# Optimization experiments

Measured on AMD Instinct MI355X. Metric: run time of the kernel, lower is better.

## Reference

```python
import jax, jax.numpy as jnp
import numpy as np

HIDDEN = 1024
N_HEADS = 16
HEAD_DIM = HIDDEN // N_HEADS


def setup_inputs() -> dict:
    key = jax.random.key(0)
    ks = jax.random.split(key, 10)
    s = 0.02
    return {
        "x": jax.random.normal(ks[0], (2, 2048, HIDDEN), dtype=jnp.float32),
        "wq_w": jax.random.normal(ks[1], (HEAD_DIM, HEAD_DIM), dtype=jnp.float32) * s,
        "wq_b": jax.random.normal(ks[2], (HEAD_DIM,), dtype=jnp.float32) * s,
        "wk_w": jax.random.normal(ks[3], (HEAD_DIM, HEAD_DIM), dtype=jnp.float32) * s,
        "wk_b": jax.random.normal(ks[4], (HEAD_DIM,), dtype=jnp.float32) * s,
        "wv_w": jax.random.normal(ks[5], (HEAD_DIM, HEAD_DIM), dtype=jnp.float32) * s,
        "wv_b": jax.random.normal(ks[6], (HEAD_DIM,), dtype=jnp.float32) * s,
        "wo_w": jax.random.normal(ks[7], (HIDDEN, HIDDEN), dtype=jnp.float32) * s,
        "wo_b": jax.random.normal(ks[8], (HIDDEN,), dtype=jnp.float32) * s,
    }


def reference(x, wq_w, wq_b, wk_w, wk_b, wv_w, wv_b, wo_w, wo_b):
    B, S, _ = x.shape
    # Faithful to torch: plain reshape (view), NOT a transpose-based head split.
    xh = x.reshape(B, N_HEADS, S, HEAD_DIM)  # [B,H,S,D]
    # torch Linear: y = x @ W.T + b
    Q = jnp.einsum('bhsd,ed->bhse', xh, wq_w) + wq_b
    K = jnp.einsum('bhsd,ed->bhse', xh, wk_w) + wk_b
    V = jnp.einsum('bhsd,ed->bhse', xh, wv_w) + wv_b
    scale = 1.0 / jnp.sqrt(jnp.float32(HEAD_DIM))
    scores = jnp.einsum('bhqd,bhkd->bhqk', Q, K) * scale  # [B,H,S,S]
    attn = jax.nn.softmax(scores, axis=-1)
    ctx = jnp.einsum('bhqk,bhkd->bhqd', attn, V)  # [B,H,S,D]
    out = ctx.reshape(B, S, HIDDEN)
    return out @ wo_w.T + wo_b
```

## Files before the change

### kernel.cpp

```cpp
#include <hip/hip_runtime.h>
#include <hip/hip_bf16.h>

#define SEQ 2048
#define BHCOUNT 32
#define NROWS (BHCOUNT*SEQ)

typedef unsigned short u16;
typedef unsigned int u32;
using bf16x8 = __attribute__((ext_vector_type(8))) short;
using f32x4  = __attribute__((ext_vector_type(4))) float;

__device__ __forceinline__ float bf2f(u16 h) {
    return __uint_as_float(((u32)h) << 16);
}
__device__ __forceinline__ u16 f2bf(float f) {
    u32 u = __float_as_uint(f);
    u32 r = (u + 0x7FFFu + ((u >> 16) & 1u)) >> 16;
    return (u16)r;
}
__device__ __forceinline__ float fexp2(float x) {
    float r; asm("v_exp_f32 %0, %1" : "=v"(r) : "v"(x)); return r;
}

__device__ __forceinline__ void gload16(const u16* g, u16* l) {
    __builtin_amdgcn_global_load_lds(
        (const __attribute__((address_space(1))) u32*)g,
        (__attribute__((address_space(3))) u32*)l, 16, 0, 0);
}

__device__ __forceinline__ void cvt8(const float* src, float sc, u16* o) {
    float4 a = *(const float4*)src;
    float4 b = *(const float4*)(src + 4);
    o[0]=f2bf(a.x*sc); o[1]=f2bf(a.y*sc); o[2]=f2bf(a.z*sc); o[3]=f2bf(a.w*sc);
    o[4]=f2bf(b.x*sc); o[5]=f2bf(b.y*sc); o[6]=f2bf(b.z*sc); o[7]=f2bf(b.w*sc);
}

__global__ __launch_bounds__(256) void qkv_kernel(
    const float* __restrict__ x,
    const float* __restrict__ wq, const float* __restrict__ bq,
    const float* __restrict__ wk, const float* __restrict__ bk,
    const float* __restrict__ wv, const float* __restrict__ bv,
    u16* __restrict__ Q, u16* __restrict__ K, u16* __restrict__ Vg)
{
    __shared__ u16 xs[128*64];
    __shared__ u16 ws[192*64];
    __shared__ float bs[192];
    const int t = threadIdx.x;
    const int wid = t >> 6, lane = t & 63;
    const int ln = lane & 15, g4 = lane >> 4;
    const int blk = blockIdx.x;
    const int m0 = blk * 128;
    const int bh = blk >> 4;
    const int ktg0 = (blk & 15) * 2;
    const float qscale = 0.125f * 1.44269504f;

    #pragma unroll
    for (int c = 0; c < 6; ++c) {
        int slot = c*256 + t;
        int row = slot >> 3, ks = slot & 7;
        const float* wsrc = (c < 2) ? wq : (c < 4) ? wk : wv;
        float sc = (c < 2) ? qscale : 1.f;
        u16 o[8];
        cvt8(&wsrc[(row & 63)*64 + ks*8], sc, o);
        *(uint4*)&ws[row*64 + ((ks ^ (row & 7)) << 3)] = *(uint4*)o;
    }
    #pragma unroll
    for (int c = 0; c < 4; ++c) {
        int slot = c*256 + t;
        int row = slot >> 3, ks = slot & 7;
        u16 o[8];
        cvt8(&x[(size_t)(m0 + row)*64 + ks*8], 1.f, o);
        *(uint4*)&xs[row*64 + ((ks ^ (row & 7)) << 3)] = *(uint4*)o;
    }
    if (t < 192) {
        int p = t >> 6, e = t & 63;
        bs[t] = (p == 0) ? bq[e]*qscale : (p == 1) ? bk[e] : bv[e];
    }
    __syncthreads();

    bf16x8 af[2][2];
    #pragma unroll
    for (int mf = 0; mf < 2; ++mf)
        #pragma unroll
        for (int kf = 0; kf < 2; ++kf) {
            int arow = wid*32 + mf*16 + ln;
            af[mf][kf] = *(const bf16x8*)&xs[arow*64 + (((kf*4 + g4) ^ (arow & 7)) << 3)];
        }

    #pragma unroll
    for (int p = 0; p < 2; ++p) {
        bf16x8 bfr[4][2];
        #pragma unroll
        for (int nt = 0; nt < 4; ++nt)
            #pragma unroll
            for (int kf = 0; kf < 2; ++kf) {
                int brow = p*64 + nt*16 + ln;
                bfr[nt][kf] = *(const bf16x8*)&ws[brow*64 + (((kf*4 + g4) ^ (ln & 7)) << 3)];
            }
        f32x4 acc[2][4];
        #pragma unroll
        for (int mf = 0; mf < 2; ++mf)
            #pragma unroll
            for (int nt = 0; nt < 4; ++nt) acc[mf][nt] = (f32x4){0.f,0.f,0.f,0.f};
        #pragma unroll
        for (int kf = 0; kf < 2; ++kf)
            #pragma unroll
            for (int mf = 0; mf < 2; ++mf)
                #pragma unroll
                for (int nt = 0; nt < 4; ++nt)
                    acc[mf][nt] = __builtin_amdgcn_mfma_f32_16x16x32_bf16(
                        af[mf][kf], bfr[nt][kf], acc[mf][nt], 0, 0, 0);
        u16* dst = p ? K : Q;
        #pragma unroll
        for (int mf = 0; mf < 2; ++mf)
            #pragma unroll
            for (int nt = 0; nt < 4; ++nt) {
                float bv4 = bs[p*64 + nt*16 + ln];
                #pragma unroll
                for (int r = 0; r < 4; ++r)
                    dst[(size_t)(m0 + wid*32 + mf*16 + g4*4 + r)*64 + nt*16 + ln]
                        = f2bf(acc[mf][nt][r] + bv4);
            }
    }

    bf16x8 wvf[4][2];
    #pragma unroll
    for (int et = 0; et < 4; ++et)
        #pragma unroll
        for (int kf = 0; kf < 2; ++kf) {
            int brow = 128 + et*16 + ln;
            wvf[et][kf] = *(const bf16x8*)&ws[brow*64 + (((kf*4 + g4) ^ (ln & 7)) << 3)];
        }
    f32x4 vacc[4][2];
    #pragma unroll
    for (int et = 0; et < 4; ++et)
        #pragma unroll
        for (int st = 0; st < 2; ++st) vacc[et][st] = (f32x4){0.f,0.f,0.f,0.f};
    #pragma unroll
    for (int kf = 0; kf < 2; ++kf)
        #pragma unroll
        for (int et = 0; et < 4; ++et)
            #pragma unroll
            for (int st = 0; st < 2; ++st)
                vacc[et][st] = __builtin_amdgcn_mfma_f32_16x16x32_bf16(
                    wvf[et][kf], af[st][kf], vacc[et][st], 0, 0, 0);

    __syncthreads();
    u16* vstage = xs;
    #pragma unroll
    for (int et = 0; et < 4; ++et)
        #pragma unroll
        for (int st = 0; st < 2; ++st)
            #pragma unroll
            for (int r = 0; r < 4; ++r) {
                int e = et*16 + g4*4 + r;
                int s = wid*32 + st*16 + ln;
                vstage[e*128 + ((s + 2*e) & 127)] = f2bf(vacc[et][st][r] + bs[128 + e]);
            }
    __syncthreads();

    #pragma unroll
    for (int c = 0; c < 8; ++c) {
        int j = c*256 + t;
        int kt2 = j >> 10, within = j & 1023;
        int ee = within >> 4, kp0 = (within & 15) * 4;
        int sbase = ((kp0 & 4) << 3) | ((kp0 & 32) >> 1) | ((kp0 & 24) >> 1);
        u16 o[4];
        #pragma unroll
        for (int i = 0; i < 4; ++i)
            o[i] = vstage[ee*128 + ((kt2*64 + sbase + i + 2*ee) & 127)];
        *(uint2*)&Vg[((size_t)bh*32 + ktg0 + kt2)*4096 + ee*64 + kp0] = *(uint2*)o;
    }
}

__device__ __forceinline__ void qkt_tile(
    const u16* Ks, const int (&foff)[4][2], const bf16x8 (&qf)[2], f32x4 (&sacc)[4])
{
    __builtin_amdgcn_s_setprio(1);
    #pragma unroll
    for (int nt = 0; nt < 4; ++nt) {
        sacc[nt] = (f32x4){0.f, 0.f, 0.f, 0.f};
        #pragma unroll
        for (int kf = 0; kf < 2; ++kf)
            sacc[nt] = __builtin_amdgcn_mfma_f32_16x16x32_bf16(
                *(const bf16x8*)&Ks[foff[nt][kf]], qf[kf], sacc[nt], 0, 0, 0);
    }
    __builtin_amdgcn_s_setprio(0);
}

__device__ __forceinline__ void sm_pv(
    f32x4 (&sacc)[4], f32x4 (&oacc)[4], f32x4& lacc,
    const u16* Vts, const int (&foff)[4][2], const bf16x8& ones)
{
    #pragma unroll
    for (int nt = 0; nt < 4; ++nt)
        #pragma unroll
        for (int r = 0; r < 4; ++r)
            sacc[nt][r] = fexp2(sacc[nt][r]);

    union PU { u32 w[4]; bf16x8 v; } pu0, pu1;
    asm("v_cvt_pk_bf16_f32 %0, %1, %2" : "=v"(pu0.w[0]) : "v"(sacc[0][0]), "v"(sacc[0][1]));
    asm("v_cvt_pk_bf16_f32 %0, %1, %2" : "=v"(pu0.w[1]) : "v"(sacc[0][2]), "v"(sacc[0][3]));
    asm("v_cvt_pk_bf16_f32 %0, %1, %2" : "=v"(pu0.w[2]) : "v"(sacc[2][0]), "v"(sacc[2][1]));
    asm("v_cvt_pk_bf16_f32 %0, %1, %2" : "=v"(pu0.w[3]) : "v"(sacc[2][2]), "v"(sacc[2][3]));
    asm("v_cvt_pk_bf16_f32 %0, %1, %2" : "=v"(pu1.w[0]) : "v"(sacc[1][0]), "v"(sacc[1][1]));
    asm("v_cvt_pk_bf16_f32 %0, %1, %2" : "=v"(pu1.w[1]) : "v"(sacc[1][2]), "v"(sacc[1][3]));
    asm("v_cvt_pk_bf16_f32 %0, %1, %2" : "=v"(pu1.w[2]) : "v"(sacc[3][0]), "v"(sacc[3][1]));
    asm("v_cvt_pk_bf16_f32 %0, %1, %2" : "=v"(pu1.w[3]) : "v"(sacc[3][2]), "v"(sacc[3][3]));
    bf16x8 pf[2] = { pu0.v, pu1.v };

    __builtin_amdgcn_s_setprio(1);
    #pragma unroll
    for (int dt = 0; dt < 4; ++dt)
        #pragma unroll
        for (int kf = 0; kf < 2; ++kf)
            oacc[dt] = __builtin_amdgcn_mfma_f32_16x16x32_bf16(
                pf[kf], *(const bf16x8*)&Vts[foff[dt][kf]], oacc[dt], 0, 0, 0);
    #pragma unroll
    for (int kf = 0; kf < 2; ++kf)
        lacc = __builtin_amdgcn_mfma_f32_16x16x32_bf16(pf[kf], ones, lacc, 0, 0, 0);
    __builtin_amdgcn_s_setprio(0);
}

__global__ __launch_bounds__(512) void attn_kernel(
    const u16* __restrict__ Q, const u16* __restrict__ K,
    const u16* __restrict__ Vg, u16* __restrict__ ctx)
{
    __shared__ u16 Kls[3*4096];
    __shared__ u16 Vls[3*4096];

    const int t = threadIdx.x;
    const int wid = t >> 6, lane = t & 63;
    const int ln = lane & 15, g4 = lane >> 4;
    const int bh = blockIdx.y;
    const size_t base   = (size_t)bh * SEQ * 64;
    const size_t vgbase = (size_t)bh * 32 * 4096;
    const int q0 = blockIdx.x * 128 + wid * 16;

    int goff;
    {
        int row = t >> 3, ks = t & 7;
        goff = row*64 + ((ks ^ (row & 7)) << 3);
    }
    const int ldst = wid * 512;

    int foff[4][2];
    #pragma unroll
    for (int nt = 0; nt < 4; ++nt)
        #pragma unroll
        for (int kf = 0; kf < 2; ++kf) {
            int frow = nt*16 + ln;
            foff[nt][kf] = frow*64 + (((kf*4 + g4) ^ (frow & 7)) << 3);
        }

    bf16x8 qf[2];
    #pragma unroll
    for (int kf = 0; kf < 2; ++kf)
        qf[kf] = *(const bf16x8*)&Q[base + (size_t)(q0 + ln)*64 + kf*32 + g4*8];

    bf16x8 ones;
    #pragma unroll
    for (int i = 0; i < 8; ++i) ones[i] = (short)0x3F80;

    f32x4 oacc[4];
    #pragma unroll
    for (int i = 0; i < 4; ++i) oacc[i] = (f32x4){0.f, 0.f, 0.f, 0.f};
    f32x4 lacc = (f32x4){0.f, 0.f, 0.f, 0.f};

    gload16(&K [base   + goff], &Kls[ldst]);
    gload16(&Vg[vgbase + goff], &Vls[ldst]);
    gload16(&K [base   + 4096 + goff], &Kls[4096 + ldst]);
    gload16(&Vg[vgbase + 4096 + goff], &Vls[4096 + ldst]);
    const u16* kptr = &K [base   + 2*4096 + goff];
    const u16* vptr = &Vg[vgbase + 2*4096 + goff];
    __syncthreads();

    f32x4 sA[4], sB[4];
    qkt_tile(&Kls[0], foff, qf, sA);

    #define ABODY(PREV, CUR, SP, SC, SN, STG)                               \
        do {                                                                \
            __syncthreads();                                                \
            if (STG) {                                                      \
                gload16(kptr, &Kls[(SN)*4096 + ldst]);                      \
                gload16(vptr, &Vls[(SN)*4096 + ldst]);                      \
                kptr += 4096; vptr += 4096;                                 \
            }                                                               \
            qkt_tile(&Kls[(SC)*4096], foff, qf, CUR);                       \
            sm_pv(PREV, oacc, lacc, &Vls[(SP)*4096], foff, ones);           \
        } while (0)

    for (int c = 0; c < 5; ++c) {
        ABODY(sA, sB, 0, 1, 2, 1);
        ABODY(sB, sA, 1, 2, 0, 1);
        ABODY(sA, sB, 2, 0, 1, 1);
        ABODY(sB, sA, 0, 1, 2, 1);
        ABODY(sA, sB, 1, 2, 0, 1);
        ABODY(sB, sA, 2, 0, 1, 1);
    }
    ABODY(sA, sB, 0, 1, 2, 0);
    sm_pv(sB, oacc, lacc, &Vls[1*4096], foff, ones);

    #undef ABODY

    #pragma unroll
    for (int r = 0; r < 4; ++r) {
        float inv = 1.f / lacc[r];
        size_t row = base + (size_t)(q0 + g4*4 + r)*64;
        #pragma unroll
        for (int dt = 0; dt < 4; ++dt)
            ctx[row + dt*16 + ln] = f2bf(oacc[dt][r] * inv);
    }
}

__global__ __launch_bounds__(256) void wconv_kernel(
    const float* __restrict__ wo, u16* __restrict__ wob_t)
{
    int g = blockIdx.x*256 + threadIdx.x;
    int tile = g >> 9, within = g & 511;
    int row = within >> 3, ks = within & 7;
    int cb = tile >> 4, kt = tile & 15;
    u16 o[8];
    cvt8(&wo[(size_t)(cb*64 + row)*1024 + kt*64 + ks*8], 1.f, o);
    *(uint4*)&wob_t[(size_t)g*8] = *(uint4*)o;
}

__global__ __launch_bounds__(256) void oproj_kernel(
    const u16* __restrict__ ctx, const u16* __restrict__ wob_t,
    const float* __restrict__ bo, float* __restrict__ out)
{
    __shared__ u16 As[128*64];
    __shared__ u16 Bs[64*64];
    const int t = threadIdx.x;
    const int wid = t >> 6, lane = t & 63;
    const int ln = lane & 15, g4 = lane >> 4;
    const int wr = wid >> 1, wc = wid & 1;
    const int rb = blockIdx.x, cb = blockIdx.y;
    const int m0 = rb * 128;

    f32x4 acc[4][2];
    #pragma unroll
    for (int mf = 0; mf < 4; ++mf)
        #pragma unroll
        for (int nf = 0; nf < 2; ++nf)
            acc[mf][nf] = (f32x4){0.f, 0.f, 0.f, 0.f};

    for (int kt = 0; kt < 16; ++kt) {
        const u16* bsrc = &wob_t[(size_t)(cb*16 + kt) * 4096];
        __syncthreads();
        #pragma unroll
        for (int c = 0; c < 4; ++c) {
            int sA = t + c*256;
            int row = sA >> 3, ks = sA & 7;
            *(uint4*)&As[row*64 + ((ks ^ (row & 7)) << 3)] =
                *(const uint4*)&ctx[(size_t)(m0 + row)*1024 + kt*64 + ks*8];
        }
        #pragma unroll
        for (int c = 0; c < 2; ++c) {
            int sB = t + c*256;
            int row = sB >> 3, ks = sB & 7;
            *(uint4*)&Bs[row*64 + ((ks ^ (row & 7)) << 3)] = *(const uint4*)&bsrc[sB*8];
        }
        __syncthreads();

        #pragma unroll
        for (int kf = 0; kf < 2; ++kf) {
            bf16x8 af[4], bfr[2];
            #pragma unroll
            for (int mf = 0; mf < 4; ++mf) {
                int arow = wr*64 + mf*16 + ln;
                af[mf] = *(const bf16x8*)&As[arow*64 + (((kf*4 + g4) ^ (arow & 7)) << 3)];
            }
            #pragma unroll
            for (int nf = 0; nf < 2; ++nf) {
                int brow = wc*32 + nf*16 + ln;
                bfr[nf] = *(const bf16x8*)&Bs[brow*64 + (((kf*4 + g4) ^ (brow & 7)) << 3)];
            }
            #pragma unroll
            for (int mf = 0; mf < 4; ++mf)
                #pragma unroll
                for (int nf = 0; nf < 2; ++nf)
                    acc[mf][nf] = __builtin_amdgcn_mfma_f32_16x16x32_bf16(af[mf], bfr[nf], acc[mf][nf], 0, 0, 0);
        }
    }

    #pragma unroll
    for (int mf = 0; mf < 4; ++mf)
        #pragma unroll
        for (int r = 0; r < 4; ++r) {
            int m = m0 + wr*64 + mf*16 + g4*4 + r;
            #pragma unroll
            for (int nf = 0; nf < 2; ++nf) {
                int col = cb*64 + wc*32 + nf*16 + ln;
                out[(size_t)m*1024 + col] = acc[mf][nf][r] + bo[col];
            }
        }
}

extern "C" void kernel_launch(void* const* d_in, const int* in_sizes, int n_in,
                              void* d_out, int out_size, void* d_ws, size_t ws_size,
                              hipStream_t stream) {
    (void)in_sizes; (void)n_in; (void)out_size; (void)ws_size;
    const float* x  = (const float*)d_in[0];
    const float* wq = (const float*)d_in[1];
    const float* bq = (const float*)d_in[2];
    const float* wk = (const float*)d_in[3];
    const float* bk = (const float*)d_in[4];
    const float* wv = (const float*)d_in[5];
    const float* bv = (const float*)d_in[6];
    const float* wo = (const float*)d_in[7];
    const float* bo = (const float*)d_in[8];
    float* out = (float*)d_out;

    u16* Qb  = (u16*)d_ws;
    u16* Kb  = Qb + (size_t)NROWS*64;
    u16* Vgb = Kb + (size_t)NROWS*64;
    u16* ctx = Vgb + (size_t)NROWS*64;
    u16* wob_t = Qb;

    qkv_kernel<<<dim3(NROWS/128), 256, 0, stream>>>(x, wq, bq, wk, bk, wv, bv, Qb, Kb, Vgb);
    attn_kernel<<<dim3(16, 32), 512, 0, stream>>>(Qb, Kb, Vgb, ctx);
    wconv_kernel<<<dim3(512), 256, 0, stream>>>(wo, wob_t);
    oproj_kernel<<<dim3(32, 16), 256, 0, stream>>>(ctx, wob_t, bo, out);
}
```

Measured before the change: 74.81 us.

## Fold wo conversion into QKV launch and double-buffer oproj with async LDS loads

The separate wconv kernel is merged into the QKV kernel as 512 extra blocks, which removes one launch. Its output buffer moves to its own workspace region after ctx, so it is no longer aliased with Q. The output-projection GEMM now uses double-buffered LDS filled by global_load_lds direct loads with a pre-swizzled global addressing. The next k-tile is prefetched while MFMAs run on the current one, and s_setprio is raised around the math. The cost is twice the LDS in oproj and extra workspace for wob_t.

Result: faster. 71.40 us (-4.6%).

```diff
diff --git a/kernel.cpp b/kernel.cpp
--- a/kernel.cpp
+++ b/kernel.cpp
@@ -35,17 +35,31 @@
     o[4]=f2bf(b.x*sc); o[5]=f2bf(b.y*sc); o[6]=f2bf(b.z*sc); o[7]=f2bf(b.w*sc);
 }
 
-__global__ __launch_bounds__(256) void qkv_kernel(
+__global__ __launch_bounds__(256) void qkv_wconv_kernel(
     const float* __restrict__ x,
     const float* __restrict__ wq, const float* __restrict__ bq,
     const float* __restrict__ wk, const float* __restrict__ bk,
     const float* __restrict__ wv, const float* __restrict__ bv,
-    u16* __restrict__ Q, u16* __restrict__ K, u16* __restrict__ Vg)
+    const float* __restrict__ wo,
+    u16* __restrict__ Q, u16* __restrict__ K, u16* __restrict__ Vg,
+    u16* __restrict__ wob_t)
 {
     __shared__ u16 xs[128*64];
     __shared__ u16 ws[192*64];
     __shared__ float bs[192];
     const int t = threadIdx.x;
+
+    if (blockIdx.x >= 512) {
+        int g = (blockIdx.x - 512)*256 + t;
+        int tile = g >> 9, within = g & 511;
+        int row = within >> 3, ks = within & 7;
+        int cb = tile >> 4, kt = tile & 15;
+        u16 o[8];
+        cvt8(&wo[(size_t)(cb*64 + row)*1024 + kt*64 + ks*8], 1.f, o);
+        *(uint4*)&wob_t[(size_t)g*8] = *(uint4*)o;
+        return;
+    }
+
     const int wid = t >> 6, lane = t & 63;
     const int ln = lane & 15, g4 = lane >> 4;
     const int blk = blockIdx.x;
@@ -313,24 +327,12 @@
     }
 }
 
-__global__ __launch_bounds__(256) void wconv_kernel(
-    const float* __restrict__ wo, u16* __restrict__ wob_t)
-{
-    int g = blockIdx.x*256 + threadIdx.x;
-    int tile = g >> 9, within = g & 511;
-    int row = within >> 3, ks = within & 7;
-    int cb = tile >> 4, kt = tile & 15;
-    u16 o[8];
-    cvt8(&wo[(size_t)(cb*64 + row)*1024 + kt*64 + ks*8], 1.f, o);
-    *(uint4*)&wob_t[(size_t)g*8] = *(uint4*)o;
-}
-
 __global__ __launch_bounds__(256) void oproj_kernel(
     const u16* __restrict__ ctx, const u16* __restrict__ wob_t,
     const float* __restrict__ bo, float* __restrict__ out)
 {
-    __shared__ u16 As[128*64];
-    __shared__ u16 Bs[64*64];
+    __shared__ u16 Als[2][128*64];
+    __shared__ u16 Bls[2][64*64];
     const int t = threadIdx.x;
     const int wid = t >> 6, lane = t & 63;
     const int ln = lane & 15, g4 = lane >> 4;
@@ -338,6 +340,22 @@
     const int rb = blockIdx.x, cb = blockIdx.y;
     const int m0 = rb * 128;
 
+    int gA[4], gB[2];
+    #pragma unroll
+    for (int c = 0; c < 4; ++c) {
+        int slot = c*256 + t;
+        int row = slot >> 3, ks = slot & 7;
+        gA[c] = row*1024 + ((ks ^ (row & 7)) << 3);
+    }
+    #pragma unroll
+    for (int c = 0; c < 2; ++c) {
+        int slot = c*256 + t;
+        int row = slot >> 3, ks = slot & 7;
+        gB[c] = row*64 + ((ks ^ (row & 7)) << 3);
+    }
+    const u16* actx = ctx + (size_t)m0*1024;
+    const u16* bw   = wob_t + (size_t)cb*16*4096;
+
     f32x4 acc[4][2];
     #pragma unroll
     for (int mf = 0; mf < 4; ++mf)
@@ -345,42 +363,51 @@
         for (int nf = 0; nf < 2; ++nf)
             acc[mf][nf] = (f32x4){0.f, 0.f, 0.f, 0.f};
 
-    for (int kt = 0; kt < 16; ++kt) {
-        const u16* bsrc = &wob_t[(size_t)(cb*16 + kt) * 4096];
-        __syncthreads();
-        #pragma unroll
-        for (int c = 0; c < 4; ++c) {
-            int sA = t + c*256;
-            int row = sA >> 3, ks = sA & 7;
-            *(uint4*)&As[row*64 + ((ks ^ (row & 7)) << 3)] =
-                *(const uint4*)&ctx[(size_t)(m0 + row)*1024 + kt*64 + ks*8];
-        }
-        #pragma unroll
-        for (int c = 0; c < 2; ++c) {
-            int sB = t + c*256;
-            int row = sB >> 3, ks = sB & 7;
-            *(uint4*)&Bs[row*64 + ((ks ^ (row & 7)) << 3)] = *(const uint4*)&bsrc[sB*8];
-        }
-        __syncthreads();
-
-        #pragma unroll
-        for (int kf = 0; kf < 2; ++kf) {
-            bf16x8 af[4], bfr[2];
-            #pragma unroll
-            for (int mf = 0; mf < 4; ++mf) {
-                int arow = wr*64 + mf*16 + ln;
-                af[mf] = *(const bf16x8*)&As[arow*64 + (((kf*4 + g4) ^ (arow & 7)) << 3)];
-            }
-            #pragma unroll
-            for (int nf = 0; nf < 2; ++nf) {
-                int brow = wc*32 + nf*16 + ln;
-                bfr[nf] = *(const bf16x8*)&Bs[brow*64 + (((kf*4 + g4) ^ (brow & 7)) << 3)];
-            }
-            #pragma unroll
-            for (int mf = 0; mf < 4; ++mf)
-                #pragma unroll
-                for (int nf = 0; nf < 2; ++nf)
-                    acc[mf][nf] = __builtin_amdgcn_mfma_f32_16x16x32_bf16(af[mf], bfr[nf], acc[mf][nf], 0, 0, 0);
+    #pragma unroll
+    for (int c = 0; c < 4; ++c) gload16(&actx[gA[c]], &Als[0][(c*256+t)*8]);
+    #pragma unroll
+    for (int c = 0; c < 2; ++c) gload16(&bw[gB[c]],   &Bls[0][(c*256+t)*8]);
+    __syncthreads();
+
+    for (int kt2 = 0; kt2 < 8; ++kt2) {
+        #pragma unroll
+        for (int half = 0; half < 2; ++half) {
+            const int kt = kt2*2 + half;
+            if (kt < 15) {
+                #pragma unroll
+                for (int c = 0; c < 4; ++c)
+                    gload16(&actx[(kt+1)*64 + gA[c]], &Als[half^1][(c*256+t)*8]);
+                #pragma unroll
+                for (int c = 0; c < 2; ++c)
+                    gload16(&bw[(kt+1)*4096 + gB[c]], &Bls[half^1][(c*256+t)*8]);
+            }
+            const u16* As = Als[half];
+            const u16* Bs = Bls[half];
+
+            __builtin_amdgcn_s_setprio(1);
+            #pragma unroll
+            for (int kf = 0; kf < 2; ++kf) {
+                bf16x8 af[4], bfr[2];
+                #pragma unroll
+                for (int mf = 0; mf < 4; ++mf) {
+                    int arow = wr*64 + mf*16 + ln;
+                    af[mf] = *(const bf16x8*)&As[arow*64 + (((kf*4 + g4) ^ (arow & 7)) << 3)];
+                }
+                #pragma unroll
+                for (int nf = 0; nf < 2; ++nf) {
+                    int brow = wc*32 + nf*16 + ln;
+                    bfr[nf] = *(const bf16x8*)&Bs[brow*64 + (((kf*4 + g4) ^ (brow & 7)) << 3)];
+                }
+                #pragma unroll
+                for (int mf = 0; mf < 4; ++mf)
+                    #pragma unroll
+                    for (int nf = 0; nf < 2; ++nf)
+                        acc[mf][nf] = __builtin_amdgcn_mfma_f32_16x16x32_bf16(
+                            af[mf], bfr[nf], acc[mf][nf], 0, 0, 0);
+            }
+            __builtin_amdgcn_s_setprio(0);
+
+            __syncthreads();
         }
     }
 
@@ -416,10 +443,10 @@
     u16* Kb  = Qb + (size_t)NROWS*64;
     u16* Vgb = Kb + (size_t)NROWS*64;
     u16* ctx = Vgb + (size_t)NROWS*64;
-    u16* wob_t = Qb;
-
-    qkv_kernel<<<dim3(NROWS/128), 256, 0, stream>>>(x, wq, bq, wk, bk, wv, bv, Qb, Kb, Vgb);
+    u16* wob_t = ctx + (size_t)NROWS*64;
+
+    qkv_wconv_kernel<<<dim3(1024), 256, 0, stream>>>(
+        x, wq, bq, wk, bk, wv, bv, wo, Qb, Kb, Vgb, wob_t);
     attn_kernel<<<dim3(16, 32), 512, 0, stream>>>(Qb, Kb, Vgb, ctx);
-    wconv_kernel<<<dim3(512), 256, 0, stream>>>(wo, wob_t);
     oproj_kernel<<<dim3(32, 16), 256, 0, stream>>>(ctx, wob_t, bo, out);
 }
```
